# Kernel tuning notes

Hardware: AMD Instinct MI355X
Metric: run time of the kernel (lower is better)

The kernel has to match this reference:

```python
import jax, jax.numpy as jnp
import numpy as np

N = 50000
E = 800000
NEG_SLOPE = 0.2
BN_EPS = 1e-5


def _gat_conv(x, src, dst, W, a_src, a_dst, bias, heads, out_ch, concat):
    # Linear projection per head: [N, heads, out_ch]
    h = (x @ W).reshape(-1, heads, out_ch)
    # Per-node attention terms alpha_src/alpha_dst: [N, heads]
    al_s = (h * a_src[None]).sum(-1)
    al_d = (h * a_dst[None]).sum(-1)
    # Edge logits with LeakyReLU: [E, heads]
    logits = jax.nn.leaky_relu(al_s[src] + al_d[dst], NEG_SLOPE)
    # Segment (scatter) softmax over edges grouped by destination node
    m = jax.ops.segment_max(logits, dst, num_segments=N)
    e = jnp.exp(logits - m[dst])
    s = jax.ops.segment_sum(e, dst, num_segments=N)
    alpha = e / (s[dst] + 1e-16)                      # [E, heads]
    # Weighted message aggregation: scatter-add to destinations
    msg = h[src] * alpha[:, :, None]                  # [E, heads, out_ch]
    out = jax.ops.segment_sum(msg, dst, num_segments=N)  # [N, heads, out_ch]
    out = out.reshape(-1, heads * out_ch) if concat else out.mean(axis=1)
    return out + bias


def _bn_eval(x, gamma, beta, mean, var):
    return (x - mean) * jax.lax.rsqrt(var + BN_EPS) * gamma + beta


def setup_inputs() -> dict:
    key = jax.random.key(0)
    ks = jax.random.split(key, 12)
    in_ch, hid, heads, out_cls = 128, 64, 2, 40
    return {
        "x": jax.random.normal(ks[0], (N, in_ch), jnp.float32),
        "edge_index": jax.random.randint(ks[1], (2, E), 0, N, jnp.int32),
        "W1": jax.random.normal(ks[2], (in_ch, heads * hid), jnp.float32) * 0.1,
        "a1_src": jax.random.normal(ks[3], (heads, hid), jnp.float32) * 0.1,
        "a1_dst": jax.random.normal(ks[4], (heads, hid), jnp.float32) * 0.1,
        "b1": jnp.zeros((heads * hid,), jnp.float32),
        "bn1_gamma": jnp.ones((heads * hid,), jnp.float32),
        "bn1_beta": jnp.zeros((heads * hid,), jnp.float32),
        "bn1_mean": jax.random.normal(ks[5], (heads * hid,), jnp.float32) * 0.1,
        "bn1_var": jax.random.uniform(ks[6], (heads * hid,), jnp.float32, 0.5, 1.5),
        "W2": jax.random.normal(ks[7], (heads * hid, out_cls), jnp.float32) * 0.1,
        "a2_src": jax.random.normal(ks[8], (1, out_cls), jnp.float32) * 0.1,
        "a2_dst": jax.random.normal(ks[9], (1, out_cls), jnp.float32) * 0.1,
        "b2": jnp.zeros((out_cls,), jnp.float32),
    }


def reference(x, edge_index, W1, a1_src, a1_dst, b1, bn1_gamma, bn1_beta,
              bn1_mean, bn1_var, W2, a2_src, a2_dst, b2):
    # add self loops
    loops = jnp.arange(N, dtype=edge_index.dtype)
    src = jnp.concatenate([edge_index[0], loops])
    dst = jnp.concatenate([edge_index[1], loops])
    # layer 1: GATConv(heads=2, concat) -> BN(eval) -> ReLU (dropout is eval no-op)
    h = _gat_conv(x, src, dst, W1, a1_src, a1_dst, b1, heads=2, out_ch=64, concat=True)
    h = jax.nn.relu(_bn_eval(h, bn1_gamma, bn1_beta, bn1_mean, bn1_var))
    # output layer: GATConv(heads=1, concat=False)
    out = _gat_conv(h, src, dst, W2, a2_src, a2_dst, b2, heads=1, out_ch=40, concat=False)
    return jax.nn.log_softmax(out, axis=1)
```

## Files before the change

kernel.cpp:

```cpp
#include <hip/hip_runtime.h>
#include <hip/hip_bf16.h>

#define NEG_SLOPE 0.2f
#define BN_EPS 1e-5f

#define NBLK 256
#define COARSE_SHIFT 9
#define COARSE_NPB 512

__device__ __forceinline__ float wred_sum(float v) {
    #pragma unroll
    for (int m = 32; m > 0; m >>= 1) v += __shfl_xor(v, m);
    return v;
}
__device__ __forceinline__ float wred_max(float v) {
    #pragma unroll
    for (int m = 32; m > 0; m >>= 1) v = fmaxf(v, __shfl_xor(v, m));
    return v;
}
__device__ __forceinline__ float xor16_sum(float v) {
    #pragma unroll
    for (int m = 1; m < 16; m <<= 1) v += __shfl_xor(v, m);
    return v;
}

__device__ __forceinline__ unsigned pack_bf16(float a, float b) {
    __hip_bfloat162 t;
    t.x = __float2bfloat16(a);
    t.y = __float2bfloat16(b);
    return *(unsigned*)&t;
}
__device__ __forceinline__ float2 unpack_bf16(unsigned u) {
    __hip_bfloat162 t = *(__hip_bfloat162*)&u;
    return {__bfloat162float(t.x), __bfloat162float(t.y)};
}

__device__ __forceinline__ unsigned enc_ord(float f) {
    unsigned u = __float_as_uint(f);
    return (u & 0x80000000u) ? ~u : (u | 0x80000000u);
}
__device__ __forceinline__ float dec_ord(unsigned e) {
    unsigned u = (e & 0x80000000u) ? (e ^ 0x80000000u) : ~e;
    return __uint_as_float(u);
}

__global__ __launch_bounds__(256) void part_hist(const int* __restrict__ ei, int E, int Et,
                                                 int chunk, int* __restrict__ hist, int nCoarse) {
    __shared__ int h[128];
    int b = blockIdx.x, t = threadIdx.x;
    if (t < 128) h[t] = 0;
    __syncthreads();
    int beg = b * chunk, end = min(beg + chunk, Et);
    for (int idx = beg + t; idx < end; idx += 256) {
        int d = (idx < E) ? ei[E + idx] : (idx - E);
        atomicAdd(&h[d >> COARSE_SHIFT], 1);
    }
    __syncthreads();
    if (t < nCoarse) hist[t * NBLK + b] = h[t];
}

__global__ __launch_bounds__(256) void coarse_total(const int* __restrict__ hist,
                                                    int* __restrict__ ctot) {
    __shared__ int red[256];
    int c = blockIdx.x, t = threadIdx.x;
    red[t] = hist[c * NBLK + t];
    __syncthreads();
    for (int off = 128; off > 0; off >>= 1) {
        if (t < off) red[t] += red[t + off];
        __syncthreads();
    }
    if (t == 0) ctot[c] = red[0];
}

__global__ __launch_bounds__(128) void coarse_scan(const int* __restrict__ ctot,
                                                   int* __restrict__ cbase, int nCoarse) {
    __shared__ int s[128];
    int t = threadIdx.x;
    int v = (t < nCoarse) ? ctot[t] : 0;
    s[t] = v;
    __syncthreads();
    for (int off = 1; off < 128; off <<= 1) {
        int u = (t >= off) ? s[t - off] : 0;
        __syncthreads();
        s[t] += u;
        __syncthreads();
    }
    if (t < nCoarse) cbase[t] = s[t] - v;
    if (t == 127) cbase[nCoarse] = s[127];
}

__global__ __launch_bounds__(64) void part_scan(int* __restrict__ hist,
                                                const int* __restrict__ cbase, int nCoarse) {
    int c = blockIdx.x, t = threadIdx.x;
    int base = cbase[c];
    int idx = c * NBLK + 4 * t;
    int4 v = *(int4*)&hist[idx];
    int sl = v.x + v.y + v.z + v.w;
    int inc = sl;
    #pragma unroll
    for (int off = 1; off < 64; off <<= 1) {
        int u = __shfl_up(inc, off);
        if (t >= off) inc += u;
    }
    int exc = inc - sl + base;
    int4 o;
    o.x = exc;
    o.y = exc + v.x;
    o.z = exc + v.x + v.y;
    o.w = exc + v.x + v.y + v.z;
    *(int4*)&hist[idx] = o;
}

__global__ __launch_bounds__(256) void part_scatter(const int* __restrict__ ei, int E, int Et,
                                                    int chunk, const int* __restrict__ hist,
                                                    unsigned* __restrict__ staged, int nCoarse) {
    __shared__ int cur[128];
    int b = blockIdx.x, t = threadIdx.x;
    if (t < nCoarse) cur[t] = hist[t * NBLK + b];
    __syncthreads();
    int beg = b * chunk, end = min(beg + chunk, Et);
    for (int idx = beg + t; idx < end; idx += 256) {
        int s, d;
        if (idx < E) { s = ei[idx]; d = ei[E + idx]; }
        else         { s = idx - E; d = idx - E; }
        int c = d >> COARSE_SHIFT;
        int pos = atomicAdd(&cur[c], 1);
        staged[pos] = ((unsigned)s << COARSE_SHIFT) | (unsigned)(d & (COARSE_NPB - 1));
    }
}

__global__ __launch_bounds__(512) void fine_place(const unsigned* __restrict__ staged,
                                                  const int* __restrict__ cbase,
                                                  int* __restrict__ offs,
                                                  int* __restrict__ csr, int Nn, int nCoarse) {
    __shared__ int hcnt[COARSE_NPB];
    __shared__ int scn[COARSE_NPB];
    int b = blockIdx.x, t = threadIdx.x;
    int node0 = b << COARSE_SHIFT;
    int nloc = min(COARSE_NPB, Nn - node0);
    hcnt[t] = 0;
    __syncthreads();
    int ebeg = cbase[b], eend = cbase[b + 1];
    for (int p = ebeg + t; p < eend; p += 512) {
        atomicAdd(&hcnt[staged[p] & (COARSE_NPB - 1)], 1);
    }
    __syncthreads();
    int val = hcnt[t];
    scn[t] = val;
    __syncthreads();
    for (int off = 1; off < COARSE_NPB; off <<= 1) {
        int u = (t >= off) ? scn[t - off] : 0;
        __syncthreads();
        scn[t] += u;
        __syncthreads();
    }
    int exc = ebeg + scn[t] - val;
    if (t < nloc) offs[node0 + t] = exc;
    if (b == nCoarse - 1 && t == 0) offs[Nn] = eend;
    hcnt[t] = exc;
    __syncthreads();
    for (int p = ebeg + t; p < eend; p += 512) {
        unsigned v = staged[p];
        int pos = atomicAdd(&hcnt[v & (COARSE_NPB - 1)], 1);
        csr[pos] = (int)(v >> COARSE_SHIFT);
    }
}

__global__ __launch_bounds__(256) void gemm1_tiled(const float* __restrict__ x,
                                                   const float* __restrict__ W,
                                                   const float* __restrict__ a1s,
                                                   const float* __restrict__ a1d,
                                                   unsigned* __restrict__ h1b,
                                                   float* __restrict__ als,
                                                   float* __restrict__ ald, int Nn) {
    __shared__ float Ast[32][132];
    __shared__ float Bs[32][132];
    int t  = threadIdx.x;
    int tx = t & 15;
    int ty = t >> 4;
    int br = blockIdx.x * 128;

    float acc[8][8];
    #pragma unroll
    for (int i = 0; i < 8; ++i)
        #pragma unroll
        for (int j = 0; j < 8; ++j) acc[i][j] = 0.f;

    int k4   = t & 7;
    int rowA = t >> 3;

    for (int k0 = 0; k0 < 128; k0 += 32) {
        #pragma unroll
        for (int i = 0; i < 4; ++i) {
            int r  = rowA + 32 * i;
            int gr = min(br + r, Nn - 1);
            float4 v = *(const float4*)(x + (size_t)gr * 128 + k0 + 4 * k4);
            Ast[4 * k4 + 0][r] = v.x; Ast[4 * k4 + 1][r] = v.y;
            Ast[4 * k4 + 2][r] = v.z; Ast[4 * k4 + 3][r] = v.w;
        }
        #pragma unroll
        for (int i = 0; i < 4; ++i) {
            int f  = t + 256 * i;
            int kk = f >> 5, c4 = f & 31;
            *(float4*)&Bs[kk][4 * c4] = *(const float4*)(W + (size_t)(k0 + kk) * 128 + 4 * c4);
        }
        __syncthreads();
        #pragma unroll 8
        for (int kk = 0; kk < 32; ++kk) {
            float4 a0 = *(const float4*)&Ast[kk][8 * ty];
            float4 a1 = *(const float4*)&Ast[kk][8 * ty + 4];
            float4 b0 = *(const float4*)&Bs[kk][8 * tx];
            float4 b1 = *(const float4*)&Bs[kk][8 * tx + 4];
            float av[8] = {a0.x, a0.y, a0.z, a0.w, a1.x, a1.y, a1.z, a1.w};
            float bv[8] = {b0.x, b0.y, b0.z, b0.w, b1.x, b1.y, b1.z, b1.w};
            #pragma unroll
            for (int i = 0; i < 8; ++i)
                #pragma unroll
                for (int j = 0; j < 8; ++j) acc[i][j] += av[i] * bv[j];
        }
        __syncthreads();
    }

    float a_s[8], a_d[8];
    #pragma unroll
    for (int j = 0; j < 8; ++j) { a_s[j] = a1s[8 * tx + j]; a_d[j] = a1d[8 * tx + j]; }
    bool h0 = (tx < 8);

    #pragma unroll
    for (int i = 0; i < 8; ++i) {
        int r = br + 8 * ty + i;
        if (r < Nn) {
            uint4 pk;
            pk.x = pack_bf16(acc[i][0], acc[i][1]);
            pk.y = pack_bf16(acc[i][2], acc[i][3]);
            pk.z = pack_bf16(acc[i][4], acc[i][5]);
            pk.w = pack_bf16(acc[i][6], acc[i][7]);
            *(uint4*)(h1b + (size_t)r * 64 + 4 * tx) = pk;
        }
        float ps = 0.f, pd = 0.f;
        #pragma unroll
        for (int j = 0; j < 8; ++j) { ps += acc[i][j] * a_s[j]; pd += acc[i][j] * a_d[j]; }
        float s0 = xor16_sum(h0 ? ps : 0.f);
        float s1 = xor16_sum(h0 ? 0.f : ps);
        float d0 = xor16_sum(h0 ? pd : 0.f);
        float d1 = xor16_sum(h0 ? 0.f : pd);
        if (tx == 0 && r < Nn) {
            als[r * 2] = s0; als[r * 2 + 1] = s1;
            ald[r * 2] = d0; ald[r * 2 + 1] = d1;
        }
    }
}

template <int H>
__global__ __launch_bounds__(256) void almax_kernel(const float* __restrict__ als,
                                                    unsigned* __restrict__ gmax, int off, int Nn,
                                                    const float* __restrict__ b1,
                                                    const float* __restrict__ g1,
                                                    const float* __restrict__ be1,
                                                    const float* __restrict__ mn1,
                                                    const float* __restrict__ vr1,
                                                    float* __restrict__ bnscale,
                                                    float* __restrict__ bnshift) {
    __shared__ float red[4][H];
    int t = threadIdx.x;
    if (bnscale && blockIdx.x == 0 && t < 128) {
        float sc = rsqrtf(vr1[t] + BN_EPS) * g1[t];
        bnscale[t] = sc;
        bnshift[t] = be1[t] + (b1[t] - mn1[t]) * sc;
    }
    float m[H];
    #pragma unroll
    for (int h = 0; h < H; ++h) m[h] = -1e30f;
    for (int n = blockIdx.x * 256 + t; n < Nn; n += gridDim.x * 256) {
        #pragma unroll
        for (int h = 0; h < H; ++h) m[h] = fmaxf(m[h], als[n * H + h]);
    }
    #pragma unroll
    for (int h = 0; h < H; ++h) m[h] = wred_max(m[h]);
    int wid = t >> 6;
    if ((t & 63) == 0) {
        #pragma unroll
        for (int h = 0; h < H; ++h) red[wid][h] = m[h];
    }
    __syncthreads();
    if (t == 0) {
        #pragma unroll
        for (int h = 0; h < H; ++h) {
            float mm = fmaxf(fmaxf(red[0][h], red[1][h]), fmaxf(red[2][h], red[3][h]));
            atomicMax(&gmax[off + h], enc_ord(mm));
        }
    }
}

__global__ __launch_bounds__(256) void softagg1_kernel(const int* __restrict__ offs, const int* __restrict__ csr,
                            const unsigned* __restrict__ h1b,
                            const float* __restrict__ als, const float* __restrict__ ald,
                            const unsigned* __restrict__ gmax,
                            const float* __restrict__ bnscale, const float* __restrict__ bnshift,
                            float* __restrict__ hbn, int Nn) {
    __shared__ int   sh_s[4][64];
    __shared__ float sh_e0[4][64];
    __shared__ float sh_e1[4][64];
    int wid = threadIdx.x >> 6, lane = threadIdx.x & 63;
    int n = blockIdx.x * 4 + wid;
    if (n >= Nn) return;
    int b = offs[n], e = offs[n + 1];
    float2 aldn = *(const float2*)(ald + n * 2);
    float bd0 = dec_ord(gmax[0]) + aldn.x; bd0 = (bd0 > 0.f) ? bd0 : NEG_SLOPE * bd0;
    float bd1 = dec_ord(gmax[1]) + aldn.y; bd1 = (bd1 > 0.f) ? bd1 : NEG_SLOPE * bd1;

    int eslot = lane >> 3;
    int l8    = lane & 7;
    float acc[16];
    #pragma unroll
    for (int j = 0; j < 16; ++j) acc[j] = 0.f;
    float den0 = 0.f, den1 = 0.f;

    for (int base = b; base < e; base += 64) {
        int cnt = min(64, e - base);
        int   s1 = 0;
        float e0r = 0.f, e1r = 0.f;
        if (lane < cnt) {
            s1 = csr[base + lane];
            float2 as = *(const float2*)(als + (size_t)s1 * 2);
            float l0 = as.x + aldn.x; l0 = (l0 > 0.f) ? l0 : NEG_SLOPE * l0;
            float l1 = as.y + aldn.y; l1 = (l1 > 0.f) ? l1 : NEG_SLOPE * l1;
            e0r = __expf(l0 - bd0);
            e1r = __expf(l1 - bd1);
            den0 += e0r; den1 += e1r;
        }
        sh_s[wid][lane]  = s1;
        sh_e0[wid][lane] = e0r;
        sh_e1[wid][lane] = e1r;
        for (int i = eslot; i < cnt; i += 8) {
            int   s  = sh_s[wid][i];
            float e0 = sh_e0[wid][i];
            float e1 = sh_e1[wid][i];
            uint4 va = *(const uint4*)(h1b + (size_t)s * 64 + 4 * l8);
            uint4 vb = *(const uint4*)(h1b + (size_t)s * 64 + 32 + 4 * l8);
            float2 f;
            f = unpack_bf16(va.x); acc[0]  += f.x * e0; acc[1]  += f.y * e0;
            f = unpack_bf16(va.y); acc[2]  += f.x * e0; acc[3]  += f.y * e0;
            f = unpack_bf16(va.z); acc[4]  += f.x * e0; acc[5]  += f.y * e0;
            f = unpack_bf16(va.w); acc[6]  += f.x * e0; acc[7]  += f.y * e0;
            f = unpack_bf16(vb.x); acc[8]  += f.x * e1; acc[9]  += f.y * e1;
            f = unpack_bf16(vb.y); acc[10] += f.x * e1; acc[11] += f.y * e1;
            f = unpack_bf16(vb.z); acc[12] += f.x * e1; acc[13] += f.y * e1;
            f = unpack_bf16(vb.w); acc[14] += f.x * e1; acc[15] += f.y * e1;
        }
    }
    #pragma unroll
    for (int j = 0; j < 16; ++j) {
        acc[j] += __shfl_xor(acc[j], 8);
        acc[j] += __shfl_xor(acc[j], 16);
        acc[j] += __shfl_xor(acc[j], 32);
    }
    den0 = wred_sum(den0);
    den1 = wred_sum(den1);
    if (eslot == 0) {
        float inv0 = 1.f / (den0 + 1e-16f);
        float inv1 = 1.f / (den1 + 1e-16f);
        int c0 = 8 * l8, c1 = 64 + 8 * l8;
        float4 sa = *(const float4*)(bnscale + c0), sb = *(const float4*)(bnscale + c0 + 4);
        float4 ha = *(const float4*)(bnshift + c0), hb = *(const float4*)(bnshift + c0 + 4);
        float4 oa, ob;
        oa.x = fmaxf(acc[0] * inv0 * sa.x + ha.x, 0.f);
        oa.y = fmaxf(acc[1] * inv0 * sa.y + ha.y, 0.f);
        oa.z = fmaxf(acc[2] * inv0 * sa.z + ha.z, 0.f);
        oa.w = fmaxf(acc[3] * inv0 * sa.w + ha.w, 0.f);
        ob.x = fmaxf(acc[4] * inv0 * sb.x + hb.x, 0.f);
        ob.y = fmaxf(acc[5] * inv0 * sb.y + hb.y, 0.f);
        ob.z = fmaxf(acc[6] * inv0 * sb.z + hb.z, 0.f);
        ob.w = fmaxf(acc[7] * inv0 * sb.w + hb.w, 0.f);
        *(float4*)(hbn + (size_t)n * 128 + c0)     = oa;
        *(float4*)(hbn + (size_t)n * 128 + c0 + 4) = ob;
        float4 sc = *(const float4*)(bnscale + c1), sd = *(const float4*)(bnscale + c1 + 4);
        float4 hc = *(const float4*)(bnshift + c1), hd = *(const float4*)(bnshift + c1 + 4);
        float4 oc, od;
        oc.x = fmaxf(acc[8]  * inv1 * sc.x + hc.x, 0.f);
        oc.y = fmaxf(acc[9]  * inv1 * sc.y + hc.y, 0.f);
        oc.z = fmaxf(acc[10] * inv1 * sc.z + hc.z, 0.f);
        oc.w = fmaxf(acc[11] * inv1 * sc.w + hc.w, 0.f);
        od.x = fmaxf(acc[12] * inv1 * sd.x + hd.x, 0.f);
        od.y = fmaxf(acc[13] * inv1 * sd.y + hd.y, 0.f);
        od.z = fmaxf(acc[14] * inv1 * sd.z + hd.z, 0.f);
        od.w = fmaxf(acc[15] * inv1 * sd.w + hd.w, 0.f);
        *(float4*)(hbn + (size_t)n * 128 + c1)     = oc;
        *(float4*)(hbn + (size_t)n * 128 + c1 + 4) = od;
    }
}

__global__ __launch_bounds__(256) void gemm2_tiled(const float* __restrict__ hbn,
                                                   const float* __restrict__ W2,
                                                   const float* __restrict__ a2s,
                                                   const float* __restrict__ a2d,
                                                   unsigned* __restrict__ h2b,
                                                   float* __restrict__ als, float* __restrict__ ald,
                                                   int Nn) {
    __shared__ float Ast[32][132];
    __shared__ float Bs[32][68];
    int t  = threadIdx.x;
    int tx = t & 15;
    int ty = t >> 4;
    int br = blockIdx.x * 128;

    float as4[4], ad4[4];
    #pragma unroll
    for (int j = 0; j < 4; ++j) {
        int c = 4 * tx + j;
        as4[j] = (c < 40) ? a2s[c] : 0.f;
        ad4[j] = (c < 40) ? a2d[c] : 0.f;
    }

    float acc[8][4];
    #pragma unroll
    for (int i = 0; i < 8; ++i)
        #pragma unroll
        for (int j = 0; j < 4; ++j) acc[i][j] = 0.f;

    int k4   = t & 7;
    int rowA = t >> 3;

    for (int k0 = 0; k0 < 128; k0 += 32) {
        #pragma unroll
        for (int i = 0; i < 4; ++i) {
            int r  = rowA + 32 * i;
            int gr = min(br + r, Nn - 1);
            float4 v = *(const float4*)(hbn + (size_t)gr * 128 + k0 + 4 * k4);
            Ast[4 * k4 + 0][r] = v.x; Ast[4 * k4 + 1][r] = v.y;
            Ast[4 * k4 + 2][r] = v.z; Ast[4 * k4 + 3][r] = v.w;
        }
        #pragma unroll
        for (int i = 0; i < 2; ++i) {
            int f  = t + 256 * i;
            int kk = f >> 4, c4 = f & 15;
            float4 v = {0.f, 0.f, 0.f, 0.f};
            if (c4 < 10) v = *(const float4*)(W2 + (size_t)(k0 + kk) * 40 + 4 * c4);
            *(float4*)&Bs[kk][4 * c4] = v;
        }
        __syncthreads();
        #pragma unroll 8
        for (int kk = 0; kk < 32; ++kk) {
            float4 a0 = *(const float4*)&Ast[kk][8 * ty];
            float4 a1 = *(const float4*)&Ast[kk][8 * ty + 4];
            float4 b0 = *(const float4*)&Bs[kk][4 * tx];
            float av[8] = {a0.x, a0.y, a0.z, a0.w, a1.x, a1.y, a1.z, a1.w};
            #pragma unroll
            for (int i = 0; i < 8; ++i) {
                acc[i][0] += av[i] * b0.x; acc[i][1] += av[i] * b0.y;
                acc[i][2] += av[i] * b0.z; acc[i][3] += av[i] * b0.w;
            }
        }
        __syncthreads();
    }

    #pragma unroll
    for (int i = 0; i < 8; ++i) {
        int r = br + 8 * ty + i;
        if (r < Nn) {
            uint2 pk = {pack_bf16(acc[i][0], acc[i][1]), pack_bf16(acc[i][2], acc[i][3])};
            *(uint2*)(h2b + (size_t)r * 32 + 2 * tx) = pk;
        }
        float ps = acc[i][0] * as4[0] + acc[i][1] * as4[1] + acc[i][2] * as4[2] + acc[i][3] * as4[3];
        float pd = acc[i][0] * ad4[0] + acc[i][1] * ad4[1] + acc[i][2] * ad4[2] + acc[i][3] * ad4[3];
        float sS = xor16_sum(ps);
        float sD = xor16_sum(pd);
        if (tx == 0 && r < Nn) { als[r] = sS; ald[r] = sD; }
    }
}

__global__ __launch_bounds__(256) void softagg2_kernel(const int* __restrict__ offs, const int* __restrict__ csr,
                            const unsigned* __restrict__ h2b,
                            const float* __restrict__ als, const float* __restrict__ ald,
                            const unsigned* __restrict__ gmax,
                            const float* __restrict__ b2,
                            float* __restrict__ out, int Nn) {
    __shared__ int   sh_s[4][64];
    __shared__ float sh_ev[4][64];
    int wid = threadIdx.x >> 6, lane = threadIdx.x & 63;
    int n = blockIdx.x * 4 + wid;
    if (n >= Nn) return;
    int b = offs[n], e = offs[n + 1];
    float aldn = ald[n];
    float bound = dec_ord(gmax[2]) + aldn;
    bound = (bound > 0.f) ? bound : NEG_SLOPE * bound;

    int eslot = lane >> 3;
    int l8    = lane & 7;
    float acc[8];
    #pragma unroll
    for (int j = 0; j < 8; ++j) acc[j] = 0.f;
    float den = 0.f;

    for (int base = b; base < e; base += 64) {
        int cnt = min(64, e - base);
        int   s1 = 0;
        float evr = 0.f;
        if (lane < cnt) {
            s1 = csr[base + lane];
            float l = als[s1] + aldn;
            l = (l > 0.f) ? l : NEG_SLOPE * l;
            evr = __expf(l - bound);
            den += evr;
        }
        sh_s[wid][lane]  = s1;
        sh_ev[wid][lane] = evr;
        for (int i = eslot; i < cnt; i += 8) {
            int   s  = sh_s[wid][i];
            float ev = sh_ev[wid][i];
            uint4 v = *(const uint4*)(h2b + (size_t)s * 32 + 4 * l8);
            float2 f;
            f = unpack_bf16(v.x); acc[0] += f.x * ev; acc[1] += f.y * ev;
            f = unpack_bf16(v.y); acc[2] += f.x * ev; acc[3] += f.y * ev;
            f = unpack_bf16(v.z); acc[4] += f.x * ev; acc[5] += f.y * ev;
            f = unpack_bf16(v.w); acc[6] += f.x * ev; acc[7] += f.y * ev;
        }
    }
    #pragma unroll
    for (int j = 0; j < 8; ++j) {
        acc[j] += __shfl_xor(acc[j], 8);
        acc[j] += __shfl_xor(acc[j], 16);
        acc[j] += __shfl_xor(acc[j], 32);
    }
    den = wred_sum(den);
    float inv = 1.f / (den + 1e-16f);
    bool valid = (eslot == 0) && (l8 < 5);
    float vv[8];
    float lmax = -1e30f;
    if (valid) {
        int c = 8 * l8;
        #pragma unroll
        for (int j = 0; j < 8; ++j) {
            vv[j] = acc[j] * inv + b2[c + j];
            lmax = fmaxf(lmax, vv[j]);
        }
    }
    float m = wred_max(lmax);
    float es = 0.f;
    if (valid) {
        #pragma unroll
        for (int j = 0; j < 8; ++j) es += __expf(vv[j] - m);
    }
    float ssum = wred_sum(es);
    float lse = m + logf(ssum);
    if (valid) {
        float4 oa = {vv[0] - lse, vv[1] - lse, vv[2] - lse, vv[3] - lse};
        float4 ob = {vv[4] - lse, vv[5] - lse, vv[6] - lse, vv[7] - lse};
        *(float4*)(out + (size_t)n * 40 + 8 * l8)     = oa;
        *(float4*)(out + (size_t)n * 40 + 8 * l8 + 4) = ob;
    }
}

extern "C" void kernel_launch(void* const* d_in, const int* in_sizes, int n_in,
                              void* d_out, int out_size, void* d_ws, size_t ws_size,
                              hipStream_t stream) {
    const float* x    = (const float*)d_in[0];
    const int*   ei   = (const int*)d_in[1];
    const float* W1   = (const float*)d_in[2];
    const float* a1s  = (const float*)d_in[3];
    const float* a1d  = (const float*)d_in[4];
    const float* b1   = (const float*)d_in[5];
    const float* g1   = (const float*)d_in[6];
    const float* be1  = (const float*)d_in[7];
    const float* mn1  = (const float*)d_in[8];
    const float* vr1  = (const float*)d_in[9];
    const float* W2   = (const float*)d_in[10];
    const float* a2s  = (const float*)d_in[11];
    const float* a2d  = (const float*)d_in[12];
    const float* b2   = (const float*)d_in[13];
    float* out = (float*)d_out;

    const int N  = in_sizes[0] / 128;
    const int E  = in_sizes[1] / 2;
    const int Et = E + N;
    const int nCoarse = (N + COARSE_NPB - 1) >> COARSE_SHIFT;
    const int chunk   = (Et + NBLK - 1) / NBLK;

    char* p = (char*)d_ws;
    auto alloc = [&](size_t bytes) -> void* {
        void* r = (void*)p;
        p += (bytes + 255) & ~(size_t)255;
        return r;
    };
    int*      hist   = (int*)alloc((size_t)nCoarse * NBLK * 4);
    int*      ctot   = (int*)alloc((size_t)nCoarse * 4);
    int*      cbase  = (int*)alloc((size_t)(nCoarse + 1) * 4);
    int*      offs   = (int*)alloc((size_t)(N + 1) * 4);
    unsigned* staged = (unsigned*)alloc((size_t)Et * 4);
    int*      csr    = (int*)alloc((size_t)Et * 4);
    unsigned* h1b    = (unsigned*)alloc((size_t)N * 64 * 4);
    float*    al1sv  = (float*)alloc((size_t)N * 2 * 4);
    float*    al1dv  = (float*)alloc((size_t)N * 2 * 4);
    float*    hbn    = (float*)alloc((size_t)N * 128 * 4);
    unsigned* h2b    = (unsigned*)alloc((size_t)N * 32 * 4);
    float*    al2sv  = (float*)alloc((size_t)N * 4);
    float*    al2dv  = (float*)alloc((size_t)N * 4);
    unsigned* gmax   = (unsigned*)alloc(4 * 4);
    float*    bnscale= (float*)alloc(128 * 4);
    float*    bnshift= (float*)alloc(128 * 4);
    (void)ws_size;

    hipMemsetAsync(gmax, 0, 16, stream);

    part_hist<<<NBLK, 256, 0, stream>>>(ei, E, Et, chunk, hist, nCoarse);
    coarse_total<<<nCoarse, 256, 0, stream>>>(hist, ctot);
    coarse_scan<<<1, 128, 0, stream>>>(ctot, cbase, nCoarse);
    part_scan<<<nCoarse, 64, 0, stream>>>(hist, cbase, nCoarse);
    part_scatter<<<NBLK, 256, 0, stream>>>(ei, E, Et, chunk, hist, staged, nCoarse);
    fine_place<<<nCoarse, 512, 0, stream>>>(staged, cbase, offs, csr, N, nCoarse);

    gemm1_tiled<<<(N + 127) / 128, 256, 0, stream>>>(x, W1, a1s, a1d, h1b, al1sv, al1dv, N);
    almax_kernel<2><<<64, 256, 0, stream>>>(al1sv, gmax, 0, N, b1, g1, be1, mn1, vr1, bnscale, bnshift);
    softagg1_kernel<<<(N + 3) / 4, 256, 0, stream>>>(offs, csr, h1b, al1sv, al1dv, gmax,
                                                     bnscale, bnshift, hbn, N);

    gemm2_tiled<<<(N + 127) / 128, 256, 0, stream>>>(hbn, W2, a2s, a2d, h2b, al2sv, al2dv, N);
    almax_kernel<1><<<64, 256, 0, stream>>>(al2sv, gmax, 2, N, nullptr, nullptr, nullptr, nullptr,
                                            nullptr, nullptr, nullptr);
    softagg2_kernel<<<(N + 3) / 4, 256, 0, stream>>>(offs, csr, h2b, al2sv, al2dv, gmax, b2, out, N);
}
```

Measured before the change: 262.8 us.

## Store layer-1 output in bf16, unroll gathers by two, merge CSR scan kernels

The layer-1 activation buffer after BN and ReLU is now written as packed bf16, halving its write traffic in softagg1 and its read traffic in gemm2. The edge-gather loops in both aggregation kernels process two edges per iteration so more independent loads are in flight. The three small CSR scan kernels are folded into one 1024-thread block, removing two launches. Rounding the hidden activations to bf16 adds a small numerical error.

```diff
diff --git a/kernel.cpp b/kernel.cpp
--- a/kernel.cpp
+++ b/kernel.cpp
@@ -16,6 +16,11 @@
 __device__ __forceinline__ float wred_max(float v) {
     #pragma unroll
     for (int m = 32; m > 0; m >>= 1) v = fmaxf(v, __shfl_xor(v, m));
+    return v;
+}
+__device__ __forceinline__ int wred_isum(int v) {
+    #pragma unroll
+    for (int m = 32; m > 0; m >>= 1) v += __shfl_xor(v, m);
     return v;
 }
 __device__ __forceinline__ float xor16_sum(float v) {
@@ -59,56 +64,54 @@
     if (t < nCoarse) hist[t * NBLK + b] = h[t];
 }
 
-__global__ __launch_bounds__(256) void coarse_total(const int* __restrict__ hist,
-                                                    int* __restrict__ ctot) {
-    __shared__ int red[256];
-    int c = blockIdx.x, t = threadIdx.x;
-    red[t] = hist[c * NBLK + t];
-    __syncthreads();
-    for (int off = 128; off > 0; off >>= 1) {
-        if (t < off) red[t] += red[t + off];
-        __syncthreads();
-    }
-    if (t == 0) ctot[c] = red[0];
-}
-
-__global__ __launch_bounds__(128) void coarse_scan(const int* __restrict__ ctot,
-                                                   int* __restrict__ cbase, int nCoarse) {
-    __shared__ int s[128];
+__global__ __launch_bounds__(1024) void csr_mid(int* __restrict__ hist,
+                                                int* __restrict__ cbase, int nCoarse) {
+    __shared__ int ctot_s[128];
+    __shared__ int scn[128];
+    __shared__ int cb_s[129];
     int t = threadIdx.x;
-    int v = (t < nCoarse) ? ctot[t] : 0;
-    s[t] = v;
+    int wv = t >> 6, ln = t & 63;
+    if (t < 128) ctot_s[t] = 0;
+    __syncthreads();
+    for (int c = wv; c < nCoarse; c += 16) {
+        int idx = c * NBLK + 4 * ln;
+        int4 v = *(int4*)&hist[idx];
+        int s = wred_isum(v.x + v.y + v.z + v.w);
+        if (ln == 0) ctot_s[c] = s;
+    }
+    __syncthreads();
+    int v0 = 0;
+    if (t < 128) { v0 = ctot_s[t]; scn[t] = v0; }
     __syncthreads();
     for (int off = 1; off < 128; off <<= 1) {
-        int u = (t >= off) ? s[t - off] : 0;
-        __syncthreads();
-        s[t] += u;
-        __syncthreads();
-    }
-    if (t < nCoarse) cbase[t] = s[t] - v;
-    if (t == 127) cbase[nCoarse] = s[127];
-}
-
-__global__ __launch_bounds__(64) void part_scan(int* __restrict__ hist,
-                                                const int* __restrict__ cbase, int nCoarse) {
-    int c = blockIdx.x, t = threadIdx.x;
-    int base = cbase[c];
-    int idx = c * NBLK + 4 * t;
-    int4 v = *(int4*)&hist[idx];
-    int sl = v.x + v.y + v.z + v.w;
-    int inc = sl;
-    #pragma unroll
-    for (int off = 1; off < 64; off <<= 1) {
-        int u = __shfl_up(inc, off);
-        if (t >= off) inc += u;
-    }
-    int exc = inc - sl + base;
-    int4 o;
-    o.x = exc;
-    o.y = exc + v.x;
-    o.z = exc + v.x + v.y;
-    o.w = exc + v.x + v.y + v.z;
-    *(int4*)&hist[idx] = o;
+        int u = (t >= off && t < 128) ? scn[t - off] : 0;
+        __syncthreads();
+        if (t < 128) scn[t] += u;
+        __syncthreads();
+    }
+    if (t < 128) cb_s[t] = scn[t] - v0;
+    if (t == 127) cb_s[128] = scn[127];
+    __syncthreads();
+    if (t <= nCoarse) cbase[t] = cb_s[t];
+    for (int c = wv; c < nCoarse; c += 16) {
+        int base = cb_s[c];
+        int idx = c * NBLK + 4 * ln;
+        int4 v = *(int4*)&hist[idx];
+        int sl = v.x + v.y + v.z + v.w;
+        int inc = sl;
+        #pragma unroll
+        for (int off = 1; off < 64; off <<= 1) {
+            int u = __shfl_up(inc, off);
+            if (ln >= off) inc += u;
+        }
+        int exc = inc - sl + base;
+        int4 o;
+        o.x = exc;
+        o.y = exc + v.x;
+        o.z = exc + v.x + v.y;
+        o.w = exc + v.x + v.y + v.z;
+        *(int4*)&hist[idx] = o;
+    }
 }
 
 __global__ __launch_bounds__(256) void part_scatter(const int* __restrict__ ei, int E, int Et,
@@ -297,7 +300,7 @@
                             const float* __restrict__ als, const float* __restrict__ ald,
                             const unsigned* __restrict__ gmax,
                             const float* __restrict__ bnscale, const float* __restrict__ bnshift,
-                            float* __restrict__ hbn, int Nn) {
+                            unsigned* __restrict__ hbnb, int Nn) {
     __shared__ int   sh_s[4][64];
     __shared__ float sh_e0[4][64];
     __shared__ float sh_e1[4][64];
@@ -332,12 +335,42 @@
         sh_s[wid][lane]  = s1;
         sh_e0[wid][lane] = e0r;
         sh_e1[wid][lane] = e1r;
-        for (int i = eslot; i < cnt; i += 8) {
+        int i = eslot;
+        for (; i + 8 < cnt; i += 16) {
+            int   sA  = sh_s[wid][i];
+            int   sB  = sh_s[wid][i + 8];
+            float e0A = sh_e0[wid][i],  e1A = sh_e1[wid][i];
+            float e0B = sh_e0[wid][i + 8], e1B = sh_e1[wid][i + 8];
+            const uint4* pA = (const uint4*)(h1b + (size_t)sA * 64 + 4 * l8);
+            const uint4* pB = (const uint4*)(h1b + (size_t)sB * 64 + 4 * l8);
+            uint4 vaA = pA[0];
+            uint4 vbA = pA[8];
+            uint4 vaB = pB[0];
+            uint4 vbB = pB[8];
+            float2 f;
+            f = unpack_bf16(vaA.x); acc[0]  += f.x * e0A; acc[1]  += f.y * e0A;
+            f = unpack_bf16(vaA.y); acc[2]  += f.x * e0A; acc[3]  += f.y * e0A;
+            f = unpack_bf16(vaA.z); acc[4]  += f.x * e0A; acc[5]  += f.y * e0A;
+            f = unpack_bf16(vaA.w); acc[6]  += f.x * e0A; acc[7]  += f.y * e0A;
+            f = unpack_bf16(vbA.x); acc[8]  += f.x * e1A; acc[9]  += f.y * e1A;
+            f = unpack_bf16(vbA.y); acc[10] += f.x * e1A; acc[11] += f.y * e1A;
+            f = unpack_bf16(vbA.z); acc[12] += f.x * e1A; acc[13] += f.y * e1A;
+            f = unpack_bf16(vbA.w); acc[14] += f.x * e1A; acc[15] += f.y * e1A;
+            f = unpack_bf16(vaB.x); acc[0]  += f.x * e0B; acc[1]  += f.y * e0B;
+            f = unpack_bf16(vaB.y); acc[2]  += f.x * e0B; acc[3]  += f.y * e0B;
+            f = unpack_bf16(vaB.z); acc[4]  += f.x * e0B; acc[5]  += f.y * e0B;
+            f = unpack_bf16(vaB.w); acc[6]  += f.x * e0B; acc[7]  += f.y * e0B;
+            f = unpack_bf16(vbB.x); acc[8]  += f.x * e1B; acc[9]  += f.y * e1B;
+            f = unpack_bf16(vbB.y); acc[10] += f.x * e1B; acc[11] += f.y * e1B;
+            f = unpack_bf16(vbB.z); acc[12] += f.x * e1B; acc[13] += f.y * e1B;
+            f = unpack_bf16(vbB.w); acc[14] += f.x * e1B; acc[15] += f.y * e1B;
+        }
+        if (i < cnt) {
             int   s  = sh_s[wid][i];
-            float e0 = sh_e0[wid][i];
-            float e1 = sh_e1[wid][i];
-            uint4 va = *(const uint4*)(h1b + (size_t)s * 64 + 4 * l8);
-            uint4 vb = *(const uint4*)(h1b + (size_t)s * 64 + 32 + 4 * l8);
+            float e0 = sh_e0[wid][i], e1 = sh_e1[wid][i];
+            const uint4* pR = (const uint4*)(h1b + (size_t)s * 64 + 4 * l8);
+            uint4 va = pR[0];
+            uint4 vb = pR[8];
             float2 f;
             f = unpack_bf16(va.x); acc[0]  += f.x * e0; acc[1]  += f.y * e0;
             f = unpack_bf16(va.y); acc[2]  += f.x * e0; acc[3]  += f.y * e0;
@@ -363,34 +396,32 @@
         int c0 = 8 * l8, c1 = 64 + 8 * l8;
         float4 sa = *(const float4*)(bnscale + c0), sb = *(const float4*)(bnscale + c0 + 4);
         float4 ha = *(const float4*)(bnshift + c0), hb = *(const float4*)(bnshift + c0 + 4);
-        float4 oa, ob;
-        oa.x = fmaxf(acc[0] * inv0 * sa.x + ha.x, 0.f);
-        oa.y = fmaxf(acc[1] * inv0 * sa.y + ha.y, 0.f);
-        oa.z = fmaxf(acc[2] * inv0 * sa.z + ha.z, 0.f);
-        oa.w = fmaxf(acc[3] * inv0 * sa.w + ha.w, 0.f);
-        ob.x = fmaxf(acc[4] * inv0 * sb.x + hb.x, 0.f);
-        ob.y = fmaxf(acc[5] * inv0 * sb.y + hb.y, 0.f);
-        ob.z = fmaxf(acc[6] * inv0 * sb.z + hb.z, 0.f);
-        ob.w = fmaxf(acc[7] * inv0 * sb.w + hb.w, 0.f);
-        *(float4*)(hbn + (size_t)n * 128 + c0)     = oa;
-        *(float4*)(hbn + (size_t)n * 128 + c0 + 4) = ob;
+        float o0 = fmaxf(acc[0] * inv0 * sa.x + ha.x, 0.f);
+        float o1 = fmaxf(acc[1] * inv0 * sa.y + ha.y, 0.f);
+        float o2 = fmaxf(acc[2] * inv0 * sa.z + ha.z, 0.f);
+        float o3 = fmaxf(acc[3] * inv0 * sa.w + ha.w, 0.f);
+        float o4 = fmaxf(acc[4] * inv0 * sb.x + hb.x, 0.f);
+        float o5 = fmaxf(acc[5] * inv0 * sb.y + hb.y, 0.f);
+        float o6 = fmaxf(acc[6] * inv0 * sb.z + hb.z, 0.f);
+        float o7 = fmaxf(acc[7] * inv0 * sb.w + hb.w, 0.f);
+        uint4 pk0 = {pack_bf16(o0, o1), pack_bf16(o2, o3), pack_bf16(o4, o5), pack_bf16(o6, o7)};
+        *(uint4*)(hbnb + (size_t)n * 64 + 4 * l8) = pk0;
         float4 sc = *(const float4*)(bnscale + c1), sd = *(const float4*)(bnscale + c1 + 4);
         float4 hc = *(const float4*)(bnshift + c1), hd = *(const float4*)(bnshift + c1 + 4);
-        float4 oc, od;
-        oc.x = fmaxf(acc[8]  * inv1 * sc.x + hc.x, 0.f);
-        oc.y = fmaxf(acc[9]  * inv1 * sc.y + hc.y, 0.f);
-        oc.z = fmaxf(acc[10] * inv1 * sc.z + hc.z, 0.f);
-        oc.w = fmaxf(acc[11] * inv1 * sc.w + hc.w, 0.f);
-        od.x = fmaxf(acc[12] * inv1 * sd.x + hd.x, 0.f);
-        od.y = fmaxf(acc[13] * inv1 * sd.y + hd.y, 0.f);
-        od.z = fmaxf(acc[14] * inv1 * sd.z + hd.z, 0.f);
-        od.w = fmaxf(acc[15] * inv1 * sd.w + hd.w, 0.f);
-        *(float4*)(hbn + (size_t)n * 128 + c1)     = oc;
-        *(float4*)(hbn + (size_t)n * 128 + c1 + 4) = od;
-    }
-}
-
-__global__ __launch_bounds__(256) void gemm2_tiled(const float* __restrict__ hbn,
+        float p0 = fmaxf(acc[8]  * inv1 * sc.x + hc.x, 0.f);
+        float p1 = fmaxf(acc[9]  * inv1 * sc.y + hc.y, 0.f);
+        float p2 = fmaxf(acc[10] * inv1 * sc.z + hc.z, 0.f);
+        float p3 = fmaxf(acc[11] * inv1 * sc.w + hc.w, 0.f);
+        float p4 = fmaxf(acc[12] * inv1 * sd.x + hd.x, 0.f);
+        float p5 = fmaxf(acc[13] * inv1 * sd.y + hd.y, 0.f);
+        float p6 = fmaxf(acc[14] * inv1 * sd.z + hd.z, 0.f);
+        float p7 = fmaxf(acc[15] * inv1 * sd.w + hd.w, 0.f);
+        uint4 pk1 = {pack_bf16(p0, p1), pack_bf16(p2, p3), pack_bf16(p4, p5), pack_bf16(p6, p7)};
+        *(uint4*)(hbnb + (size_t)n * 64 + 32 + 4 * l8) = pk1;
+    }
+}
+
+__global__ __launch_bounds__(256) void gemm2_tiled(const unsigned* __restrict__ hbnb,
                                                    const float* __restrict__ W2,
                                                    const float* __restrict__ a2s,
                                                    const float* __restrict__ a2d,
@@ -426,9 +457,10 @@
         for (int i = 0; i < 4; ++i) {
             int r  = rowA + 32 * i;
             int gr = min(br + r, Nn - 1);
-            float4 v = *(const float4*)(hbn + (size_t)gr * 128 + k0 + 4 * k4);
-            Ast[4 * k4 + 0][r] = v.x; Ast[4 * k4 + 1][r] = v.y;
-            Ast[4 * k4 + 2][r] = v.z; Ast[4 * k4 + 3][r] = v.w;
+            uint2 v2 = *(const uint2*)(hbnb + (size_t)gr * 64 + (k0 >> 1) + 2 * k4);
+            float2 f0 = unpack_bf16(v2.x), f1 = unpack_bf16(v2.y);
+            Ast[4 * k4 + 0][r] = f0.x; Ast[4 * k4 + 1][r] = f0.y;
+            Ast[4 * k4 + 2][r] = f1.x; Ast[4 * k4 + 3][r] = f1.y;
         }
         #pragma unroll
         for (int i = 0; i < 2; ++i) {
@@ -505,7 +537,25 @@
         }
         sh_s[wid][lane]  = s1;
         sh_ev[wid][lane] = evr;
-        for (int i = eslot; i < cnt; i += 8) {
+        int i = eslot;
+        for (; i + 8 < cnt; i += 16) {
+            int   sA  = sh_s[wid][i];
+            int   sB  = sh_s[wid][i + 8];
+            float evA = sh_ev[wid][i];
+            float evB = sh_ev[wid][i + 8];
+            uint4 vA = *(const uint4*)(h2b + (size_t)sA * 32 + 4 * l8);
+            uint4 vB = *(const uint4*)(h2b + (size_t)sB * 32 + 4 * l8);
+            float2 f;
+            f = unpack_bf16(vA.x); acc[0] += f.x * evA; acc[1] += f.y * evA;
+            f = unpack_bf16(vA.y); acc[2] += f.x * evA; acc[3] += f.y * evA;
+            f = unpack_bf16(vA.z); acc[4] += f.x * evA; acc[5] += f.y * evA;
+            f = unpack_bf16(vA.w); acc[6] += f.x * evA; acc[7] += f.y * evA;
+            f = unpack_bf16(vB.x); acc[0] += f.x * evB; acc[1] += f.y * evB;
+            f = unpack_bf16(vB.y); acc[2] += f.x * evB; acc[3] += f.y * evB;
+            f = unpack_bf16(vB.z); acc[4] += f.x * evB; acc[5] += f.y * evB;
+            f = unpack_bf16(vB.w); acc[6] += f.x * evB; acc[7] += f.y * evB;
+        }
+        if (i < cnt) {
             int   s  = sh_s[wid][i];
             float ev = sh_ev[wid][i];
             uint4 v = *(const uint4*)(h2b + (size_t)s * 32 + 4 * l8);
@@ -583,7 +633,6 @@
         return r;
     };
     int*      hist   = (int*)alloc((size_t)nCoarse * NBLK * 4);
-    int*      ctot   = (int*)alloc((size_t)nCoarse * 4);
     int*      cbase  = (int*)alloc((size_t)(nCoarse + 1) * 4);
     int*      offs   = (int*)alloc((size_t)(N + 1) * 4);
     unsigned* staged = (unsigned*)alloc((size_t)Et * 4);
@@ -591,7 +640,7 @@
     unsigned* h1b    = (unsigned*)alloc((size_t)N * 64 * 4);
     float*    al1sv  = (float*)alloc((size_t)N * 2 * 4);
     float*    al1dv  = (float*)alloc((size_t)N * 2 * 4);
-    float*    hbn    = (float*)alloc((size_t)N * 128 * 4);
+    unsigned* hbnb   = (unsigned*)alloc((size_t)N * 64 * 4);
     unsigned* h2b    = (unsigned*)alloc((size_t)N * 32 * 4);
     float*    al2sv  = (float*)alloc((size_t)N * 4);
     float*    al2dv  = (float*)alloc((size_t)N * 4);
@@ -603,18 +652,16 @@
     hipMemsetAsync(gmax, 0, 16, stream);
 
     part_hist<<<NBLK, 256, 0, stream>>>(ei, E, Et, chunk, hist, nCoarse);
-    coarse_total<<<nCoarse, 256, 0, stream>>>(hist, ctot);
-    coarse_scan<<<1, 128, 0, stream>>>(ctot, cbase, nCoarse);
-    part_scan<<<nCoarse, 64, 0, stream>>>(hist, cbase, nCoarse);
+    csr_mid<<<1, 1024, 0, stream>>>(hist, cbase, nCoarse);
     part_scatter<<<NBLK, 256, 0, stream>>>(ei, E, Et, chunk, hist, staged, nCoarse);
     fine_place<<<nCoarse, 512, 0, stream>>>(staged, cbase, offs, csr, N, nCoarse);
 
     gemm1_tiled<<<(N + 127) / 128, 256, 0, stream>>>(x, W1, a1s, a1d, h1b, al1sv, al1dv, N);
     almax_kernel<2><<<64, 256, 0, stream>>>(al1sv, gmax, 0, N, b1, g1, be1, mn1, vr1, bnscale, bnshift);
     softagg1_kernel<<<(N + 3) / 4, 256, 0, stream>>>(offs, csr, h1b, al1sv, al1dv, gmax,
-                                                     bnscale, bnshift, hbn, N);
-
-    gemm2_tiled<<<(N + 127) / 128, 256, 0, stream>>>(hbn, W2, a2s, a2d, h2b, al2sv, al2dv, N);
+                                                     bnscale, bnshift, hbnb, N);
+
+    gemm2_tiled<<<(N + 127) / 128, 256, 0, stream>>>(hbnb, W2, a2s, a2d, h2b, al2sv, al2dv, N);
     almax_kernel<1><<<64, 256, 0, stream>>>(al2sv, gmax, 2, N, nullptr, nullptr, nullptr, nullptr,
                                             nullptr, nullptr, nullptr);
     softagg2_kernel<<<(N + 3) / 4, 256, 0, stream>>>(offs, csr, h2b, al2sv, al2dv, gmax, b2, out, N);
```

Measured after the change: 264.9 us. About the same (+0.8%).
